# Kernel optimization log

Hardware: AMD Instinct MI355X
Metric: run time of the kernel (lower is better)

The kernel has to match this reference:

```python
import jax, jax.numpy as jnp
import numpy as np

NO_EDGE_OFFSET_T_NORM = 1.0    # added to the no_edge branch for the T-norm (min) operator
NO_EDGE_OFFSET_T_CONORM = -1.0  # added to the no_edge branch for the T-conorm (max) operator

B, IN_F, OUT_F = 2048, 256, 256
N_EDGE_TYPES, N_OPS = 2, 2


def setup_inputs() -> dict:
    key = jax.random.key(0)
    k1, k2, k3 = jax.random.split(key, 3)
    x = jax.random.uniform(k1, (B, IN_F), dtype=jnp.float32)
    prob_edge_weights = jax.random.normal(k2, (OUT_F, IN_F, N_EDGE_TYPES), dtype=jnp.float32)
    prob_node_weights = jax.random.normal(k3, (OUT_F, N_OPS), dtype=jnp.float32)
    return {"x": x, "prob_edge_weights": prob_edge_weights, "prob_node_weights": prob_node_weights}


def reference(x, prob_edge_weights, prob_node_weights):
    # train_mode = train_both: softmax over edge types and over operators
    edge_prob = jax.nn.softmax(prob_edge_weights, axis=-1)  # [O, I, E]
    node_prob = jax.nn.softmax(prob_node_weights, axis=-1)  # [O, U]

    p_edge = edge_prob[:, :, 0]     # prob of real edge (identity transform), [O, I]
    p_noedge = edge_prob[:, :, 1]   # prob of no_edge (zeros + operator-specific offset), [O, I]

    # expected edge value per (batch, out, in); the no_edge branch contributes
    # offset * p_noedge since its edge_value is zeros(x) + offset.
    base = x[:, None, :] * p_edge   # [B, O, I]

    # operator 0: T-norm (min over in_features), no_edge offset = +1
    ev_min = jnp.min(base + NO_EDGE_OFFSET_T_NORM * p_noedge, axis=-1)    # [B, O]
    # operator 1: T-conorm (max over in_features), no_edge offset = -1
    ev_max = jnp.max(base + NO_EDGE_OFFSET_T_CONORM * p_noedge, axis=-1)  # [B, O]

    # expectation over operators
    return ev_min * node_prob[:, 0] + ev_max * node_prob[:, 1]  # [B, O]
```

## Files before the change

kernel.cpp:

```cpp
#include <hip/hip_runtime.h>
#include <math.h>

#define IN_F  256
#define OUT_F 256
#define OTILE 64
#define BTILE 16
#define NTH   256

__global__ __launch_bounds__(NTH, 2)
void den_kernel(const float* __restrict__ x,
                const float* __restrict__ pew,
                const float* __restrict__ pnw,
                float* __restrict__ out)
{
    __shared__ float pe_lds[OTILE * IN_F];

    const int tid = threadIdx.x;
    const int b0  = blockIdx.x * BTILE;
    const int o0  = blockIdx.y * OTILE;

    {
        const int r16 = tid >> 4;
        const int c   = tid & 15;
        for (int rg = 0; rg < 4; ++rg) {
            const int o  = rg * 16 + r16;
            const int xm = (o & 7) << 4;
            const float4* wp = reinterpret_cast<const float4*>(pew + (size_t)(o0 + o) * (IN_F * 2));
            char* rowp = reinterpret_cast<char*>(&pe_lds[o * IN_F]);
            #pragma unroll
            for (int k = 0; k < 8; ++k) {
                float4 w = wp[k * 16 + c];
                float pe0 = __builtin_amdgcn_rcpf(1.0f + __expf(w.y - w.x));
                float pe1 = __builtin_amdgcn_rcpf(1.0f + __expf(w.w - w.z));
                const int byteoff = (8 * (k * 16 + c)) ^ xm;
                *reinterpret_cast<float2*>(rowp + byteoff) = make_float2(pe0, pe1);
            }
        }
    }
    __syncthreads();

    const int lane = tid & 63;
    const int wid  = __builtin_amdgcn_readfirstlane(tid >> 6);
    const int bb0  = b0 + wid * 4;
    const char* rowp = reinterpret_cast<const char*>(&pe_lds[lane * IN_F]);
    const int xm = (lane & 7) << 4;

    float mn[4], mx[4];
    #pragma unroll
    for (int j = 0; j < 4; ++j) { mn[j] = INFINITY; mx[j] = -INFINITY; }

    const float* xr0 = x + (size_t)bb0 * IN_F;

    #pragma unroll 4
    for (int c = 0; c < 64; ++c) {
        float4 pv = *reinterpret_cast<const float4*>(rowp + ((16 * c) ^ xm));
        #pragma unroll
        for (int j = 0; j < 4; ++j) {
            float4 xv = *reinterpret_cast<const float4*>(xr0 + j * IN_F + 4 * c);
            float t0 = __builtin_fmaf(xv.x, pv.x, -pv.x);
            float t1 = __builtin_fmaf(xv.y, pv.y, -pv.y);
            float t2 = __builtin_fmaf(xv.z, pv.z, -pv.z);
            float t3 = __builtin_fmaf(xv.w, pv.w, -pv.w);
            float u0 = __builtin_fmaf(2.0f, pv.x, t0);
            float u1 = __builtin_fmaf(2.0f, pv.y, t1);
            float u2 = __builtin_fmaf(2.0f, pv.z, t2);
            float u3 = __builtin_fmaf(2.0f, pv.w, t3);
            mn[j] = fminf(fminf(mn[j], t0), t1);
            mn[j] = fminf(fminf(mn[j], t2), t3);
            mx[j] = fmaxf(fmaxf(mx[j], u0), u1);
            mx[j] = fmaxf(fmaxf(mx[j], u2), u3);
        }
    }

    const int o = o0 + lane;
    float2 nw = *reinterpret_cast<const float2*>(pnw + 2 * (size_t)o);
    float n0 = __builtin_amdgcn_rcpf(1.0f + __expf(nw.y - nw.x));
    float n1 = 1.0f - n0;
    #pragma unroll
    for (int j = 0; j < 4; ++j) {
        out[(size_t)(bb0 + j) * OUT_F + o] = (mn[j] + 1.0f) * n0 + (mx[j] - 1.0f) * n1;
    }
}

extern "C" void kernel_launch(void* const* d_in, const int* in_sizes, int n_in,
                              void* d_out, int out_size, void* d_ws, size_t ws_size,
                              hipStream_t stream) {
    (void)d_ws; (void)ws_size; (void)n_in; (void)out_size;
    const float* x   = (const float*)d_in[0];
    const float* pew = (const float*)d_in[1];
    const float* pnw = (const float*)d_in[2];
    float* out = (float*)d_out;
    const int B = in_sizes[0] / IN_F;
    dim3 grid(B / BTILE, OUT_F / OTILE);
    den_kernel<<<grid, NTH, 0, stream>>>(x, pew, pnw, out);
}
```

Baseline: 73.13 us.

## Switch inner min/max loop to packed fp16 with half-size LDS and smaller batch tile

Stores the edge probabilities in LDS as fp16 and does the fused multiply-add and min/max on packed half2 values, which roughly halves the per-element VALU instruction count and LDS footprint. The batch tile drops from 16 to 8 and the occupancy hint rises to 4 blocks per CU, giving each wave 2 batch rows instead of 4. The risks are fp16 rounding error against the fp32 reference, extra fp32-to-fp16 conversion instructions on x, and twice as many blocks each repeating the softmax/LDS fill.

Result: slower. 77.48 us (+5.9%).

```diff
diff --git a/kernel.cpp b/kernel.cpp
--- a/kernel.cpp
+++ b/kernel.cpp
@@ -4,16 +4,18 @@
 #define IN_F  256
 #define OUT_F 256
 #define OTILE 64
-#define BTILE 16
+#define BTILE 8
 #define NTH   256
 
-__global__ __launch_bounds__(NTH, 2)
+typedef _Float16 h2 __attribute__((ext_vector_type(2)));
+
+__global__ __launch_bounds__(NTH, 4)
 void den_kernel(const float* __restrict__ x,
                 const float* __restrict__ pew,
                 const float* __restrict__ pnw,
                 float* __restrict__ out)
 {
-    __shared__ float pe_lds[OTILE * IN_F];
+    __shared__ __align__(16) _Float16 pe_lds[OTILE * IN_F];
 
     const int tid = threadIdx.x;
     const int b0  = blockIdx.x * BTILE;
@@ -24,7 +26,7 @@
         const int c   = tid & 15;
         for (int rg = 0; rg < 4; ++rg) {
             const int o  = rg * 16 + r16;
-            const int xm = (o & 7) << 4;
+            const int sw = (o & 15) << 3;
             const float4* wp = reinterpret_cast<const float4*>(pew + (size_t)(o0 + o) * (IN_F * 2));
             char* rowp = reinterpret_cast<char*>(&pe_lds[o * IN_F]);
             #pragma unroll
@@ -32,43 +34,45 @@
                 float4 w = wp[k * 16 + c];
                 float pe0 = __builtin_amdgcn_rcpf(1.0f + __expf(w.y - w.x));
                 float pe1 = __builtin_amdgcn_rcpf(1.0f + __expf(w.w - w.z));
-                const int byteoff = (8 * (k * 16 + c)) ^ xm;
-                *reinterpret_cast<float2*>(rowp + byteoff) = make_float2(pe0, pe1);
+                const int byteoff = (4 * (k * 16 + c)) ^ sw;
+                h2 pv; pv.x = (_Float16)pe0; pv.y = (_Float16)pe1;
+                *reinterpret_cast<h2*>(rowp + byteoff) = pv;
             }
         }
     }
     __syncthreads();
 
     const int lane = tid & 63;
-    const int wid  = __builtin_amdgcn_readfirstlane(tid >> 6);
-    const int bb0  = b0 + wid * 4;
+    const int wid  = tid >> 6;
+    const int bb0  = b0 + wid * 2;
     const char* rowp = reinterpret_cast<const char*>(&pe_lds[lane * IN_F]);
-    const int xm = (lane & 7) << 4;
+    const int sw = (lane & 15) << 3;
 
-    float mn[4], mx[4];
+    const h2 two2 = {(_Float16)2.0f, (_Float16)2.0f};
+    h2 mn[2], mx[2];
     #pragma unroll
-    for (int j = 0; j < 4; ++j) { mn[j] = INFINITY; mx[j] = -INFINITY; }
+    for (int j = 0; j < 2; ++j) {
+        mn[j].x = mn[j].y = (_Float16)INFINITY;
+        mx[j].x = mx[j].y = (_Float16)(-INFINITY);
+    }
 
     const float* xr0 = x + (size_t)bb0 * IN_F;
 
     #pragma unroll 4
     for (int c = 0; c < 64; ++c) {
-        float4 pv = *reinterpret_cast<const float4*>(rowp + ((16 * c) ^ xm));
+        h2 pA = *reinterpret_cast<const h2*>(rowp + ((8 * c) ^ sw));
+        h2 pB = *reinterpret_cast<const h2*>(rowp + (((8 * c) ^ sw) + 4));
         #pragma unroll
-        for (int j = 0; j < 4; ++j) {
+        for (int j = 0; j < 2; ++j) {
             float4 xv = *reinterpret_cast<const float4*>(xr0 + j * IN_F + 4 * c);
-            float t0 = __builtin_fmaf(xv.x, pv.x, -pv.x);
-            float t1 = __builtin_fmaf(xv.y, pv.y, -pv.y);
-            float t2 = __builtin_fmaf(xv.z, pv.z, -pv.z);
-            float t3 = __builtin_fmaf(xv.w, pv.w, -pv.w);
-            float u0 = __builtin_fmaf(2.0f, pv.x, t0);
-            float u1 = __builtin_fmaf(2.0f, pv.y, t1);
-            float u2 = __builtin_fmaf(2.0f, pv.z, t2);
-            float u3 = __builtin_fmaf(2.0f, pv.w, t3);
-            mn[j] = fminf(fminf(mn[j], t0), t1);
-            mn[j] = fminf(fminf(mn[j], t2), t3);
-            mx[j] = fmaxf(fmaxf(mx[j], u0), u1);
-            mx[j] = fmaxf(fmaxf(mx[j], u2), u3);
+            h2 xA; xA.x = (_Float16)xv.x; xA.y = (_Float16)xv.y;
+            h2 xB; xB.x = (_Float16)xv.z; xB.y = (_Float16)xv.w;
+            h2 tA = __builtin_elementwise_fma(xA, pA, -pA);
+            h2 tB = __builtin_elementwise_fma(xB, pB, -pB);
+            h2 uA = __builtin_elementwise_fma(two2, pA, tA);
+            h2 uB = __builtin_elementwise_fma(two2, pB, tB);
+            mn[j] = __builtin_elementwise_min(mn[j], __builtin_elementwise_min(tA, tB));
+            mx[j] = __builtin_elementwise_max(mx[j], __builtin_elementwise_max(uA, uB));
         }
     }
 
@@ -77,8 +81,10 @@
     float n0 = __builtin_amdgcn_rcpf(1.0f + __expf(nw.y - nw.x));
     float n1 = 1.0f - n0;
     #pragma unroll
-    for (int j = 0; j < 4; ++j) {
-        out[(size_t)(bb0 + j) * OUT_F + o] = (mn[j] + 1.0f) * n0 + (mx[j] - 1.0f) * n1;
+    for (int j = 0; j < 2; ++j) {
+        float mnf = fminf((float)mn[j].x, (float)mn[j].y);
+        float mxf = fmaxf((float)mx[j].x, (float)mx[j].y);
+        out[(size_t)(bb0 + j) * OUT_F + o] = (mnf + 1.0f) * n0 + (mxf - 1.0f) * n1;
     }
 }
 
```
